# Kernel tuning notes

Measured on AMD Instinct MI355X. Metric: run time of the kernel, lower is better.

## Reference

```python
import jax, jax.numpy as jnp
import numpy as np

B, L, C, H, D2 = 1, 384, 256, 8, 128
d = C // H
EPS = 1e-5
SCALE = 1.0 / np.sqrt(d).astype(np.float32)


def setup_inputs() -> dict:
    key = jax.random.key(0)
    ks = jax.random.split(key, 20)

    def lin(k, fin, fout):
        return (jax.random.normal(k, (fin, fout), jnp.float32) / np.sqrt(fin)).astype(jnp.float32)

    return {
        "x2d": jax.random.normal(ks[0], (B, L, L, D2), jnp.float32),
        "x3d": jax.random.normal(ks[1], (B, L, C), jnp.float32),
        "Wq": lin(ks[2], C, C), "bq": jax.random.normal(ks[3], (C,), jnp.float32) * 0.02,
        "Wk": lin(ks[4], C, C), "bk": jax.random.normal(ks[5], (C,), jnp.float32) * 0.02,
        "Wv": lin(ks[6], C, C), "bv": jax.random.normal(ks[7], (C,), jnp.float32) * 0.02,
        "Wpre": lin(ks[8], D2, C), "bpre": jax.random.normal(ks[9], (C,), jnp.float32) * 0.02,
        "ln_g": jnp.ones((C,), jnp.float32), "ln_b": jnp.zeros((C,), jnp.float32),
        "Weq": lin(ks[10], C, C), "beq": jax.random.normal(ks[11], (C,), jnp.float32) * 0.02,
        "Wek": lin(ks[12], C, C), "bek": jax.random.normal(ks[13], (C,), jnp.float32) * 0.02,
        "Wo": lin(ks[14], C, C), "bo": jax.random.normal(ks[15], (C,), jnp.float32) * 0.02,
    }


def reference(x2d, x3d, Wq, bq, Wk, bk, Wv, bv, Wpre, bpre, ln_g, ln_b,
              Weq, beq, Wek, bek, Wo, bo):
    def heads(x):  # (B,L,C) -> (B,H,L,d)
        return x.reshape(B, L, H, d).transpose(0, 2, 1, 3)

    q = heads(x3d @ Wq + bq)
    k = heads(x3d @ Wk + bk)
    v = heads(x3d @ Wv + bv)

    # pre_proj: Linear -> LayerNorm -> ReLU on pair features
    e = x2d @ Wpre + bpre                              # (B,L,L,C)
    mu = jnp.mean(e, axis=-1, keepdims=True)
    var = jnp.mean((e - mu) ** 2, axis=-1, keepdims=True)
    e = jax.nn.relu((e - mu) * jax.lax.rsqrt(var + EPS) * ln_g + ln_b)

    efq = (e @ Weq + beq).reshape(B, L, L, H, d)       # efq[b,i,j,h,:]
    efk = (e @ Wek + bek).reshape(B, L, L, H, d)

    # scores[b,h,i,j] = q_i.k_j + sum_d efk[b,i,j,h,d]*q[b,h,j,d], then scale
    scores = jnp.einsum('bhid,bhjd->bhij', q, k) \
           + jnp.einsum('bijhd,bhjd->bhij', efk, q)
    scores = scores * SCALE

    w = jax.nn.softmax(scores, axis=-1)
    x1 = jnp.einsum('bhij,bhjd->bhid', w, v)
    # x2[b,h,i,d] = sum_j scores[b,h,i,j] * efq[b,i,j,h,d]
    x2 = jnp.einsum('bhij,bijhd->bhid', scores, efq)

    x = (x1 + x2).transpose(0, 2, 1, 3).reshape(B, L, C)
    return x @ Wo + bo
```

## Files before the change

kernel.cpp:

```cpp
#include <hip/hip_runtime.h>
#include <hip/hip_bf16.h>

#define LLEN 384
#define CDIM 256
#define NH 8
#define HD 32
#define DIN 128
#define LN_EPS 1e-5f
#define SCL 0.17677669529663687f

typedef __attribute__((ext_vector_type(8))) short bh8;
typedef __attribute__((ext_vector_type(4))) float f32x4;
typedef __attribute__((ext_vector_type(4))) unsigned int u32x4;

__device__ __forceinline__ unsigned short f2bf(float f){
  unsigned int u = __float_as_uint(f);
  u += 0x7fffu + ((u >> 16) & 1u);
  return (unsigned short)(u >> 16);
}

__device__ __forceinline__ unsigned int pkbf(float a, float b){
#if defined(__gfx950__) && __has_builtin(__builtin_amdgcn_cvt_pk_bf16_f32)
  typedef __attribute__((ext_vector_type(2))) __bf16 vbf2;
  vbf2 v = __builtin_amdgcn_cvt_pk_bf16_f32(a, b);
  union { vbf2 v; unsigned int u; } cv; cv.v = v; return cv.u;
#else
  return (unsigned int)f2bf(a) | ((unsigned int)f2bf(b) << 16);
#endif
}

__device__ __forceinline__ float pk_reduce8(const float* v, int lane){
  bool b0 = lane & 1, b1 = lane & 2, b2 = lane & 4;
  float r0 = (b0 ? v[1] : v[0]) + __shfl_xor(b0 ? v[0] : v[1], 1, 64);
  float r1 = (b0 ? v[3] : v[2]) + __shfl_xor(b0 ? v[2] : v[3], 1, 64);
  float r2 = (b0 ? v[5] : v[4]) + __shfl_xor(b0 ? v[4] : v[5], 1, 64);
  float r3 = (b0 ? v[7] : v[6]) + __shfl_xor(b0 ? v[6] : v[7], 1, 64);
  float s0 = (b1 ? r1 : r0) + __shfl_xor(b1 ? r0 : r1, 2, 64);
  float s1 = (b1 ? r3 : r2) + __shfl_xor(b1 ? r2 : r3, 2, 64);
  float t0 = (b2 ? s1 : s0) + __shfl_xor(b2 ? s0 : s1, 4, 64);
  return t0 + __shfl_xor(t0, 8, 64);
}

__global__ __launch_bounds__(256) void pack_w(
    const float* __restrict__ Wpre, const float* __restrict__ Weq,
    const float* __restrict__ Wek,  const float* __restrict__ Wq,
    const float* __restrict__ Wk,   const float* __restrict__ Wv,
    unsigned short* __restrict__ Pp, unsigned short* __restrict__ Pq,
    unsigned short* __restrict__ Pk, unsigned short* __restrict__ PWq,
    unsigned short* __restrict__ PWk, unsigned short* __restrict__ PWv)
{
  int tid = blockIdx.x * 256 + threadIdx.x;
  const float* W; unsigned short* P; int base;
  if      (tid <  4096){ W = Wpre; P = Pp;  base = tid;         }
  else if (tid < 12288){ W = Weq;  P = Pq;  base = tid -  4096; }
  else if (tid < 20480){ W = Wek;  P = Pk;  base = tid - 12288; }
  else if (tid < 28672){ W = Wq;   P = PWq; base = tid - 20480; }
  else if (tid < 36864){ W = Wk;   P = PWk; base = tid - 28672; }
  else                 { W = Wv;   P = PWv; base = tid - 36864; }
  int l   = base & 63;
  int c   = (base >> 6) & 15;
  int kc  = base >> 10;
  int krow = kc*32 + (l >> 4)*8;
  int col  = c*16 + (l & 15);
  unsigned int wds[4];
  #pragma unroll
  for (int p = 0; p < 4; p++){
    unsigned short lo = f2bf(W[(size_t)(krow + 2*p    )*CDIM + col]);
    unsigned short hi = f2bf(W[(size_t)(krow + 2*p + 1)*CDIM + col]);
    wds[p] = (unsigned int)lo | ((unsigned int)hi << 16);
  }
  uint4 v; v.x = wds[0]; v.y = wds[1]; v.z = wds[2]; v.w = wds[3];
  *(uint4*)(P + (size_t)base*8) = v;
}

__global__ __launch_bounds__(256) void qkv_mfma(
    const float* __restrict__ x3d,
    const float* __restrict__ bq, const float* __restrict__ bk, const float* __restrict__ bv,
    const unsigned short* __restrict__ PWq, const unsigned short* __restrict__ PWk,
    const unsigned short* __restrict__ PWv,
    float* __restrict__ Vm, unsigned short* __restrict__ QmH,
    float* __restrict__ QmT, unsigned short* __restrict__ PKt)
{
  __shared__ __align__(16) unsigned short Xb[64*264];
  const int bx = blockIdx.x;
  const int jb = bx / 12, rem = bx % 12;
  const int m = rem >> 2, nq = rem & 3;
  const int t  = threadIdx.x;
  const int w  = t >> 6, l = t & 63, q4 = l >> 4, lm = l & 15;

  const float* src = x3d + (size_t)jb*64*CDIM;
  #pragma unroll
  for (int it = 0; it < 16; it++){
    int idx = it*256 + t;
    int r = idx >> 6, k4 = (idx & 63) << 2;
    float4 v = *(const float4*)(src + (size_t)r*CDIM + k4);
    ushort4 b;
    b.x = f2bf(v.x); b.y = f2bf(v.y); b.z = f2bf(v.z); b.w = f2bf(v.w);
    *(ushort4*)(&Xb[r*264 + k4]) = b;
  }
  __syncthreads();

  const unsigned short* P = (m == 0) ? PWq : (m == 1) ? PWk : PWv;
  const float* bias       = (m == 0) ? bq  : (m == 1) ? bk  : bv;
  const int cidx = nq*4 + w;
  f32x4 acc[4];
  #pragma unroll
  for (int a = 0; a < 4; a++){ f32x4 z = {0.f,0.f,0.f,0.f}; acc[a] = z; }
  #pragma unroll
  for (int kc = 0; kc < 8; kc++){
    bh8 bf = *(const bh8*)(P + ((size_t)(kc*16 + cidx)*64 + l)*8);
    #pragma unroll
    for (int rt = 0; rt < 4; rt++){
      bh8 af = *(const bh8*)(&Xb[(rt*16 + lm)*264 + kc*32 + q4*8]);
      acc[rt] = __builtin_amdgcn_mfma_f32_16x16x32_bf16(af, bf, acc[rt], 0, 0, 0);
    }
  }
  {
    int c = cidx*16 + lm;
    float bb = bias[c];
    #pragma unroll
    for (int rt = 0; rt < 4; rt++)
      #pragma unroll
      for (int rg = 0; rg < 4; rg++){
        int row = jb*64 + rt*16 + q4*4 + rg;
        float v = acc[rt][rg] + bb;
        if (m == 0){
          QmH[(size_t)row*CDIM + c] = f2bf(v);
          QmT[(size_t)c*LLEN + row] = v;
        } else if (m == 1){
          int kc2 = c >> 5;
          int jj2 = c & 7;
          int l2  = ((c >> 3) & 3)*16 + (row & 15);
          PKt[(((size_t)kc2*24 + (row >> 4))*64 + l2)*8 + jj2] = f2bf(v);
        } else {
          Vm[(size_t)row*CDIM + c] = v;
        }
      }
  }
}

__global__ __launch_bounds__(256, 4) void x3d_tiles(
  const float* __restrict__ x2d,
  const float* __restrict__ bpre, const float* __restrict__ ln_g, const float* __restrict__ ln_b,
  const float* __restrict__ beq,  const float* __restrict__ bek,
  const float* __restrict__ QmT,  const unsigned short* __restrict__ QmH,
  const unsigned short* __restrict__ PKt,
  const unsigned short* __restrict__ Pp, const unsigned short* __restrict__ Pq,
  const unsigned short* __restrict__ Pk,
  float* __restrict__ Sg, float* __restrict__ x2part)
{
  __shared__ __align__(16) unsigned short EX[64*264];
  __shared__ float rowstat[4][64][2];
  __shared__ float muS[64], istdS[64];
  __shared__ float qk1S[NH*64];

  const int bx = blockIdx.x;
  const int i = bx / 6, jt = bx % 6, j0 = jt * 64;
  const int t = threadIdx.x;
  const int w = t >> 6, l = t & 63, q4 = l >> 4, lm = l & 15;
  const int wbase = w << 6;

  bh8 aqv[2], kf[2][4];
  #pragma unroll
  for (int hh = 0; hh < 2; hh++){
    int h = 2*w + hh;
    aqv[hh] = *(const bh8*)(QmH + (size_t)i*CDIM + h*HD + q4*8);
    #pragma unroll
    for (int ct = 0; ct < 4; ct++)
      kf[hh][ct] = *(const bh8*)(PKt + (((size_t)h*24 + (jt*4 + ct))*64 + l)*8);
  }

  {
    const char* gtile = (const char*)(x2d + ((size_t)i*LLEN + j0)*DIN);
    #pragma unroll
    for (int it = 0; it < 8; it++){
      int P   = w*512 + it*64 + l;
      int row = P >> 5;
      int blk = (P & 31) ^ (row & 7);
      const void* gp = gtile + ((size_t)row*512 + ((size_t)blk << 4));
      unsigned short* lp = EX + (w*4096 + it*512);
      __builtin_amdgcn_global_load_lds(
          (const __attribute__((address_space(1))) void*)gp,
          (__attribute__((address_space(3))) void*)lp, 16, 0, 0);
    }
  }

  #pragma unroll
  for (int hh = 0; hh < 2; hh++){
    int h = 2*w + hh;
    #pragma unroll
    for (int ct = 0; ct < 4; ct++){
      f32x4 z = {0.f,0.f,0.f,0.f};
      f32x4 a1 = __builtin_amdgcn_mfma_f32_16x16x32_bf16(aqv[hh], kf[hh][ct], z, 0, 0, 0);
      if (q4 == 0) qk1S[h*64 + ct*16 + lm] = a1[0];
    }
  }

  __syncthreads();

  const float* XF = (const float*)EX;
  f32x4 acc[4][4];
  #pragma unroll
  for (int a = 0; a < 4; a++)
    #pragma unroll
    for (int b = 0; b < 4; b++){ f32x4 z = {0.f,0.f,0.f,0.f}; acc[a][b] = z; }
  #pragma unroll
  for (int kc = 0; kc < 4; kc++){
    bh8 af[4];
    #pragma unroll
    for (int rt = 0; rt < 4; rt++){
      int row = rt*16 + lm;
      int sw  = row & 7;
      int blk0 = kc*8 + q4*2;
      f32x4 a0 = *(const f32x4*)(XF + row*128 + ((blk0       ^ sw) << 2));
      f32x4 a1 = *(const f32x4*)(XF + row*128 + (((blk0 + 1) ^ sw) << 2));
      union { unsigned int u[4]; bh8 v; } cv;
      cv.u[0] = pkbf(a0[0], a0[1]); cv.u[1] = pkbf(a0[2], a0[3]);
      cv.u[2] = pkbf(a1[0], a1[1]); cv.u[3] = pkbf(a1[2], a1[3]);
      af[rt] = cv.v;
    }
    #pragma unroll
    for (int ct = 0; ct < 4; ct++){
      bh8 bf = *(const bh8*)(Pp + ((size_t)(kc*16 + (w*4 + ct))*64 + l)*8);
      #pragma unroll
      for (int rt = 0; rt < 4; rt++)
        acc[rt][ct] = __builtin_amdgcn_mfma_f32_16x16x32_bf16(af[rt], bf, acc[rt][ct], 0, 0, 0);
    }
  }

  {
    float bpre4[4];
    #pragma unroll
    for (int ct = 0; ct < 4; ct++) bpre4[ct] = bpre[wbase + ct*16 + lm];
    #pragma unroll
    for (int rt = 0; rt < 4; rt++){
      float v[8];
      #pragma unroll
      for (int p = 0; p < 8; p++) v[p] = 0.f;
      #pragma unroll
      for (int ct = 0; ct < 4; ct++){
        float bb = bpre4[ct];
        #pragma unroll
        for (int rg = 0; rg < 4; rg++){
          float x = acc[rt][ct][rg] + bb;
          acc[rt][ct][rg] = x;
          v[2*rg]   += x;
          v[2*rg+1] += x*x;
        }
      }
      float red = pk_reduce8(v, lm);
      if (lm < 8){
        int p = lm;
        rowstat[w][rt*16 + q4*4 + (p >> 1)][p & 1] = red;
      }
    }
  }
  __syncthreads();
  if (t < 64){
    float s  = rowstat[0][t][0] + rowstat[1][t][0] + rowstat[2][t][0] + rowstat[3][t][0];
    float s2 = rowstat[0][t][1] + rowstat[1][t][1] + rowstat[2][t][1] + rowstat[3][t][1];
    float mu = s * (1.f/256.f);
    float var = s2 * (1.f/256.f) - mu*mu;
    muS[t] = mu;
    istdS[t] = rsqrtf(var + LN_EPS);
  }
  __syncthreads();

  {
    float g4[4], lb4[4];
    #pragma unroll
    for (int ct = 0; ct < 4; ct++){
      int c = wbase + ct*16 + lm;
      g4[ct] = ln_g[c]; lb4[ct] = ln_b[c];
    }
    #pragma unroll
    for (int rt = 0; rt < 4; rt++){
      #pragma unroll
      for (int rg = 0; rg < 4; rg++){
        int row = rt*16 + q4*4 + rg;
        float mu = muS[row], is = istdS[row];
        #pragma unroll
        for (int ct = 0; ct < 4; ct++){
          int c = wbase + ct*16 + lm;
          float v = (acc[rt][ct][rg] - mu)*is*g4[ct] + lb4[ct];
          v = fmaxf(v, 0.f);
          EX[row*264 + c] = f2bf(v);
        }
      }
    }
  }
  __syncthreads();

  #pragma unroll
  for (int a = 0; a < 4; a++)
    #pragma unroll
    for (int b = 0; b < 4; b++){ f32x4 z = {0.f,0.f,0.f,0.f}; acc[a][b] = z; }
  #pragma unroll
  for (int kc = 0; kc < 8; kc++){
    bh8 af[4];
    #pragma unroll
    for (int rt = 0; rt < 4; rt++)
      af[rt] = *(const bh8*)(&EX[(rt*16 + lm)*264 + kc*32 + q4*8]);
    #pragma unroll
    for (int ct = 0; ct < 4; ct++){
      bh8 bf = *(const bh8*)(Pk + ((size_t)(kc*16 + (w*4 + ct))*64 + l)*8);
      #pragma unroll
      for (int rt = 0; rt < 4; rt++)
        acc[rt][ct] = __builtin_amdgcn_mfma_f32_16x16x32_bf16(af[rt], bf, acc[rt][ct], 0, 0, 0);
    }
  }

  float screg[4];
  {
    float bek4[4];
    #pragma unroll
    for (int ct = 0; ct < 4; ct++) bek4[ct] = bek[wbase + ct*16 + lm];
    #pragma unroll
    for (int rt = 0; rt < 4; rt++){
      float v[8];
      #pragma unroll
      for (int p = 0; p < 8; p++) v[p] = 0.f;
      #pragma unroll
      for (int ct = 0; ct < 4; ct++){
        float bek_ = bek4[ct];
        float4 qv = *(const float4*)(QmT + (size_t)(wbase + ct*16 + lm)*LLEN + j0 + rt*16 + q4*4);
        int wh = ct >> 1;
        v[0 + wh] += (acc[rt][ct][0] + bek_) * qv.x;
        v[2 + wh] += (acc[rt][ct][1] + bek_) * qv.y;
        v[4 + wh] += (acc[rt][ct][2] + bek_) * qv.z;
        v[6 + wh] += (acc[rt][ct][3] + bek_) * qv.w;
      }
      float red = pk_reduce8(v, lm);
      int p = lm & 7;
      int jloc = rt*16 + q4*4 + (p >> 1);
      float sc = (red + qk1S[(2*w + (p & 1))*64 + jloc]) * SCL;
      screg[rt] = sc;
      if (lm < 8)
        Sg[((size_t)i*NH + 2*w + (p & 1))*LLEN + j0 + jloc] = sc;
    }
  }

  #pragma unroll
  for (int a = 0; a < 4; a++)
    #pragma unroll
    for (int b = 0; b < 4; b++){ f32x4 z = {0.f,0.f,0.f,0.f}; acc[a][b] = z; }
  #pragma unroll
  for (int kc = 0; kc < 8; kc++){
    bh8 af[4];
    #pragma unroll
    for (int rt = 0; rt < 4; rt++)
      af[rt] = *(const bh8*)(&EX[(rt*16 + lm)*264 + kc*32 + q4*8]);
    #pragma unroll
    for (int ct = 0; ct < 4; ct++){
      bh8 bf = *(const bh8*)(Pq + ((size_t)(kc*16 + (w*4 + ct))*64 + l)*8);
      #pragma unroll
      for (int rt = 0; rt < 4; rt++)
        acc[rt][ct] = __builtin_amdgcn_mfma_f32_16x16x32_bf16(af[rt], bf, acc[rt][ct], 0, 0, 0);
    }
  }

  {
    float beq4[4];
    #pragma unroll
    for (int ct = 0; ct < 4; ct++) beq4[ct] = beq[wbase + ct*16 + lm];
    float x2p[4] = {0.f, 0.f, 0.f, 0.f};
    #pragma unroll
    for (int rt = 0; rt < 4; rt++){
      float sb[8];
      #pragma unroll
      for (int p = 0; p < 8; p++)
        sb[p] = __shfl(screg[rt], (l & 48) | p, 64);
      #pragma unroll
      for (int ct = 0; ct < 4; ct++){
        int wh = ct >> 1;
        #pragma unroll
        for (int rg = 0; rg < 4; rg++)
          x2p[ct] = fmaf(sb[2*rg + wh], acc[rt][ct][rg] + beq4[ct], x2p[ct]);
      }
    }
    bool b4 = l & 16, b5 = l & 32;
    float r0 = (b4 ? x2p[1] : x2p[0]) + __shfl_xor(b4 ? x2p[0] : x2p[1], 16, 64);
    float r1 = (b4 ? x2p[3] : x2p[2]) + __shfl_xor(b4 ? x2p[2] : x2p[3], 16, 64);
    float q  = (b5 ? r1 : r0) + __shfl_xor(b5 ? r0 : r1, 32, 64);
    int ctq = ((l >> 4) & 1) | (((l >> 5) & 1) << 1);
    x2part[((size_t)jt*LLEN + i)*CDIM + wbase + ctq*16 + lm] = q;
  }
}

__global__ __launch_bounds__(256) void finish(
    const float* __restrict__ Sg, const float* __restrict__ x2part,
    const float* __restrict__ Vm, const float* __restrict__ Wo,
    const float* __restrict__ bo, float* __restrict__ out)
{
  __shared__ float scoresS[NH*LLEN];
  __shared__ float xoutS[CDIM];
  const int i = blockIdx.x;
  const int t = threadIdx.x;

  #pragma unroll
  for (int it = 0; it < 3; it++)
    ((float4*)scoresS)[it*256 + t] = ((const float4*)(Sg + (size_t)i*NH*LLEN))[it*256 + t];
  __syncthreads();

  const int h = t >> 5;
  const int g32 = t & 31;
  float sv[12];
  float mx = -3.0e38f;
  #pragma unroll
  for (int it = 0; it < 12; it++){
    float s = scoresS[h*LLEN + it*32 + g32];
    sv[it] = s;
    mx = fmaxf(mx, s);
  }
  #pragma unroll
  for (int mk = 1; mk < 32; mk <<= 1) mx = fmaxf(mx, __shfl_xor(mx, mk, 64));
  float den = 0.f;
  #pragma unroll
  for (int it = 0; it < 12; it++){ float e = __expf(sv[it] - mx); sv[it] = e; den += e; }
  #pragma unroll
  for (int mk = 1; mk < 32; mk <<= 1) den += __shfl_xor(den, mk, 64);
  float rden = 1.f / den;
  #pragma unroll
  for (int it = 0; it < 12; it++) scoresS[h*LLEN + it*32 + g32] = sv[it]*rden;
  __syncthreads();

  float a[8];
  #pragma unroll
  for (int k = 0; k < 8; k++) a[k] = 0.f;
  {
    const float* vp = Vm + t;
    const float* sp = scoresS + h*LLEN;
    #pragma unroll 2
    for (int j = 0; j < LLEN; j += 8){
      #pragma unroll
      for (int k = 0; k < 8; k++)
        a[k] = fmaf(sp[j+k], vp[(size_t)(j+k)*CDIM], a[k]);
    }
  }
  float x1 = ((a[0]+a[1]) + (a[2]+a[3])) + ((a[4]+a[5]) + (a[6]+a[7]));
  float x2v = 0.f;
  #pragma unroll
  for (int jt = 0; jt < 6; jt++)
    x2v += x2part[((size_t)jt*LLEN + i)*CDIM + t];
  xoutS[t] = x1 + x2v;
  __syncthreads();

  float b0a = bo[t], b1a = 0.f, b2a = 0.f, b3a = 0.f;
  #pragma unroll 4
  for (int c = 0; c < CDIM; c += 4){
    b0a = fmaf(xoutS[c+0], Wo[(size_t)(c+0)*CDIM + t], b0a);
    b1a = fmaf(xoutS[c+1], Wo[(size_t)(c+1)*CDIM + t], b1a);
    b2a = fmaf(xoutS[c+2], Wo[(size_t)(c+2)*CDIM + t], b2a);
    b3a = fmaf(xoutS[c+3], Wo[(size_t)(c+3)*CDIM + t], b3a);
  }
  out[(size_t)i*CDIM + t] = (b0a + b1a) + (b2a + b3a);
}

extern "C" void kernel_launch(void* const* d_in, const int* in_sizes, int n_in,
                              void* d_out, int out_size, void* d_ws, size_t ws_size,
                              hipStream_t stream)
{
  const float* x2d  = (const float*)d_in[0];
  const float* x3d  = (const float*)d_in[1];
  const float* Wq   = (const float*)d_in[2];
  const float* bq   = (const float*)d_in[3];
  const float* Wk   = (const float*)d_in[4];
  const float* bk   = (const float*)d_in[5];
  const float* Wv   = (const float*)d_in[6];
  const float* bv   = (const float*)d_in[7];
  const float* Wpre = (const float*)d_in[8];
  const float* bpre = (const float*)d_in[9];
  const float* ln_g = (const float*)d_in[10];
  const float* ln_b = (const float*)d_in[11];
  const float* Weq  = (const float*)d_in[12];
  const float* beq  = (const float*)d_in[13];
  const float* Wek  = (const float*)d_in[14];
  const float* bek  = (const float*)d_in[15];
  const float* Wo   = (const float*)d_in[16];
  const float* bo   = (const float*)d_in[17];
  float* out = (float*)d_out;

  float* Vm  = (float*)d_ws;
  float* QmT = Vm + LLEN*CDIM;
  unsigned short* QmH = (unsigned short*)(QmT + CDIM*LLEN);
  unsigned short* PKt = QmH + LLEN*CDIM;
  unsigned short* Pp  = PKt + LLEN*CDIM;
  unsigned short* Pq  = Pp  + DIN*CDIM;
  unsigned short* Pk  = Pq  + CDIM*CDIM;
  unsigned short* PWq = Pk  + CDIM*CDIM;
  unsigned short* PWk = PWq + CDIM*CDIM;
  unsigned short* PWv = PWk + CDIM*CDIM;
  float* Sg     = (float*)(PWv + CDIM*CDIM);
  float* x2part = Sg + (size_t)LLEN*NH*LLEN;

  pack_w<<<dim3(176), dim3(256), 0, stream>>>(Wpre, Weq, Wek, Wq, Wk, Wv,
                                              Pp, Pq, Pk, PWq, PWk, PWv);
  qkv_mfma<<<dim3(72), dim3(256), 0, stream>>>(x3d, bq, bk, bv, PWq, PWk, PWv,
                                               Vm, QmH, QmT, PKt);
  x3d_tiles<<<dim3(LLEN*6), dim3(256), 0, stream>>>(x2d, bpre, ln_g, ln_b, beq, bek,
                                                    QmT, QmH, PKt, Pp, Pq, Pk, Sg, x2part);
  finish<<<dim3(LLEN), dim3(256), 0, stream>>>(Sg, x2part, Vm, Wo, bo, out);
}
```

Before: 236.5 us.

## Make x3d_tiles persistent with double-buffered LDS prefetch of next x2d tile

```diff
diff --git a/kernel.cpp b/kernel.cpp
--- a/kernel.cpp
+++ b/kernel.cpp
@@ -11,7 +11,6 @@
 
 typedef __attribute__((ext_vector_type(8))) short bh8;
 typedef __attribute__((ext_vector_type(4))) float f32x4;
-typedef __attribute__((ext_vector_type(4))) unsigned int u32x4;
 
 __device__ __forceinline__ unsigned short f2bf(float f){
   unsigned int u = __float_as_uint(f);
@@ -139,7 +138,7 @@
   }
 }
 
-__global__ __launch_bounds__(256, 4) void x3d_tiles(
+__global__ __launch_bounds__(256, 2) void x3d_tiles(
   const float* __restrict__ x2d,
   const float* __restrict__ bpre, const float* __restrict__ ln_g, const float* __restrict__ ln_b,
   const float* __restrict__ beq,  const float* __restrict__ bek,
@@ -149,89 +148,107 @@
   const unsigned short* __restrict__ Pk,
   float* __restrict__ Sg, float* __restrict__ x2part)
 {
-  __shared__ __align__(16) unsigned short EX[64*264];
+  __shared__ __align__(16) unsigned short BUF[2][64*256];
   __shared__ float rowstat[4][64][2];
   __shared__ float muS[64], istdS[64];
   __shared__ float qk1S[NH*64];
 
-  const int bx = blockIdx.x;
-  const int i = bx / 6, jt = bx % 6, j0 = jt * 64;
+  const int b = blockIdx.x;
   const int t = threadIdx.x;
   const int w = t >> 6, l = t & 63, q4 = l >> 4, lm = l & 15;
   const int wbase = w << 6;
 
-  bh8 aqv[2], kf[2][4];
-  #pragma unroll
-  for (int hh = 0; hh < 2; hh++){
-    int h = 2*w + hh;
-    aqv[hh] = *(const bh8*)(QmH + (size_t)i*CDIM + h*HD + q4*8);
-    #pragma unroll
-    for (int ct = 0; ct < 4; ct++)
-      kf[hh][ct] = *(const bh8*)(PKt + (((size_t)h*24 + (jt*4 + ct))*64 + l)*8);
-  }
-
-  {
-    const char* gtile = (const char*)(x2d + ((size_t)i*LLEN + j0)*DIN);
+  auto stage_tile = [&](int T, unsigned short* dst){
+    const int ii = T / 6, jj0 = (T % 6) * 64;
+    const char* gtile = (const char*)(x2d + ((size_t)ii*LLEN + jj0)*DIN);
     #pragma unroll
     for (int it = 0; it < 8; it++){
       int P   = w*512 + it*64 + l;
       int row = P >> 5;
       int blk = (P & 31) ^ (row & 7);
       const void* gp = gtile + ((size_t)row*512 + ((size_t)blk << 4));
-      unsigned short* lp = EX + (w*4096 + it*512);
+      unsigned short* lp = dst + (w*4096 + it*512);
       __builtin_amdgcn_global_load_lds(
           (const __attribute__((address_space(1))) void*)gp,
           (__attribute__((address_space(3))) void*)lp, 16, 0, 0);
     }
-  }
-
-  #pragma unroll
-  for (int hh = 0; hh < 2; hh++){
-    int h = 2*w + hh;
+  };
+
+  stage_tile(b, &BUF[0][0]);
+
+  int cur = 0;
+  #pragma unroll 1
+  for (int T = b; T < LLEN*6; T += 512){
+    const int i = T / 6, jt = T % 6, j0 = jt * 64;
+    unsigned short* EXs = &BUF[cur][0];
+    unsigned short* ENs = &BUF[cur ^ 1][0];
+
+    __syncthreads();
+
+    bh8 aqv[2], kf[2][4];
+    #pragma unroll
+    for (int hh = 0; hh < 2; hh++){
+      int h = 2*w + hh;
+      aqv[hh] = *(const bh8*)(QmH + (size_t)i*CDIM + h*HD + q4*8);
+      #pragma unroll
+      for (int ct = 0; ct < 4; ct++)
+        kf[hh][ct] = *(const bh8*)(PKt + (((size_t)h*24 + (jt*4 + ct))*64 + l)*8);
+    }
+    bh8 bfp[4][4];
+    #pragma unroll
+    for (int kc = 0; kc < 4; kc++)
+      #pragma unroll
+      for (int ct = 0; ct < 4; ct++)
+        bfp[kc][ct] = *(const bh8*)(Pp + ((size_t)(kc*16 + (w*4 + ct))*64 + l)*8);
+    float bpre4[4], g4[4], lb4[4];
     #pragma unroll
     for (int ct = 0; ct < 4; ct++){
-      f32x4 z = {0.f,0.f,0.f,0.f};
-      f32x4 a1 = __builtin_amdgcn_mfma_f32_16x16x32_bf16(aqv[hh], kf[hh][ct], z, 0, 0, 0);
-      if (q4 == 0) qk1S[h*64 + ct*16 + lm] = a1[0];
-    }
-  }
-
-  __syncthreads();
-
-  const float* XF = (const float*)EX;
-  f32x4 acc[4][4];
-  #pragma unroll
-  for (int a = 0; a < 4; a++)
-    #pragma unroll
-    for (int b = 0; b < 4; b++){ f32x4 z = {0.f,0.f,0.f,0.f}; acc[a][b] = z; }
-  #pragma unroll
-  for (int kc = 0; kc < 4; kc++){
-    bh8 af[4];
-    #pragma unroll
-    for (int rt = 0; rt < 4; rt++){
-      int row = rt*16 + lm;
-      int sw  = row & 7;
-      int blk0 = kc*8 + q4*2;
-      f32x4 a0 = *(const f32x4*)(XF + row*128 + ((blk0       ^ sw) << 2));
-      f32x4 a1 = *(const f32x4*)(XF + row*128 + (((blk0 + 1) ^ sw) << 2));
-      union { unsigned int u[4]; bh8 v; } cv;
-      cv.u[0] = pkbf(a0[0], a0[1]); cv.u[1] = pkbf(a0[2], a0[3]);
-      cv.u[2] = pkbf(a1[0], a1[1]); cv.u[3] = pkbf(a1[2], a1[3]);
-      af[rt] = cv.v;
-    }
-    #pragma unroll
-    for (int ct = 0; ct < 4; ct++){
-      bh8 bf = *(const bh8*)(Pp + ((size_t)(kc*16 + (w*4 + ct))*64 + l)*8);
-      #pragma unroll
-      for (int rt = 0; rt < 4; rt++)
-        acc[rt][ct] = __builtin_amdgcn_mfma_f32_16x16x32_bf16(af[rt], bf, acc[rt][ct], 0, 0, 0);
-    }
-  }
-
-  {
-    float bpre4[4];
-    #pragma unroll
-    for (int ct = 0; ct < 4; ct++) bpre4[ct] = bpre[wbase + ct*16 + lm];
+      int c = wbase + ct*16 + lm;
+      bpre4[ct] = bpre[c]; g4[ct] = ln_g[c]; lb4[ct] = ln_b[c];
+    }
+
+    if (T + 512 < LLEN*6) stage_tile(T + 512, ENs);
+
+    #pragma unroll
+    for (int hh = 0; hh < 2; hh++){
+      int h = 2*w + hh;
+      #pragma unroll
+      for (int ct = 0; ct < 4; ct++){
+        f32x4 z = {0.f,0.f,0.f,0.f};
+        f32x4 a1 = __builtin_amdgcn_mfma_f32_16x16x32_bf16(aqv[hh], kf[hh][ct], z, 0, 0, 0);
+        if (q4 == 0) qk1S[h*64 + ct*16 + lm] = a1[0];
+      }
+    }
+
+    const float* XF = (const float*)EXs;
+    f32x4 acc[4][4];
+    #pragma unroll
+    for (int a = 0; a < 4; a++)
+      #pragma unroll
+      for (int bb2 = 0; bb2 < 4; bb2++){ f32x4 z = {0.f,0.f,0.f,0.f}; acc[a][bb2] = z; }
+    #pragma unroll
+    for (int kc = 0; kc < 4; kc++){
+      bh8 af[4];
+      #pragma unroll
+      for (int rt = 0; rt < 4; rt++){
+        int row = rt*16 + lm;
+        int sw  = row & 7;
+        int blk0 = kc*8 + q4*2;
+        f32x4 a0 = *(const f32x4*)(XF + row*128 + ((blk0       ^ sw) << 2));
+        f32x4 a1 = *(const f32x4*)(XF + row*128 + (((blk0 + 1) ^ sw) << 2));
+        union { unsigned int u[4]; bh8 v; } cv;
+        cv.u[0] = pkbf(a0[0], a0[1]); cv.u[1] = pkbf(a0[2], a0[3]);
+        cv.u[2] = pkbf(a1[0], a1[1]); cv.u[3] = pkbf(a1[2], a1[3]);
+        af[rt] = cv.v;
+      }
+      #pragma unroll
+      for (int ct = 0; ct < 4; ct++){
+        #pragma unroll
+        for (int rt = 0; rt < 4; rt++)
+          acc[rt][ct] = __builtin_amdgcn_mfma_f32_16x16x32_bf16(af[rt], bfp[kc][ct], acc[rt][ct], 0, 0, 0);
+      }
+    }
+
     #pragma unroll
     for (int rt = 0; rt < 4; rt++){
       float v[8];
@@ -254,136 +271,132 @@
         rowstat[w][rt*16 + q4*4 + (p >> 1)][p & 1] = red;
       }
     }
-  }
-  __syncthreads();
-  if (t < 64){
-    float s  = rowstat[0][t][0] + rowstat[1][t][0] + rowstat[2][t][0] + rowstat[3][t][0];
-    float s2 = rowstat[0][t][1] + rowstat[1][t][1] + rowstat[2][t][1] + rowstat[3][t][1];
-    float mu = s * (1.f/256.f);
-    float var = s2 * (1.f/256.f) - mu*mu;
-    muS[t] = mu;
-    istdS[t] = rsqrtf(var + LN_EPS);
-  }
-  __syncthreads();
-
-  {
-    float g4[4], lb4[4];
-    #pragma unroll
-    for (int ct = 0; ct < 4; ct++){
-      int c = wbase + ct*16 + lm;
-      g4[ct] = ln_g[c]; lb4[ct] = ln_b[c];
-    }
+    __syncthreads();
+    if (t < 64){
+      float s  = rowstat[0][t][0] + rowstat[1][t][0] + rowstat[2][t][0] + rowstat[3][t][0];
+      float s2 = rowstat[0][t][1] + rowstat[1][t][1] + rowstat[2][t][1] + rowstat[3][t][1];
+      float mu = s * (1.f/256.f);
+      float var = s2 * (1.f/256.f) - mu*mu;
+      muS[t] = mu;
+      istdS[t] = rsqrtf(var + LN_EPS);
+    }
+    __syncthreads();
+
     #pragma unroll
     for (int rt = 0; rt < 4; rt++){
       #pragma unroll
       for (int rg = 0; rg < 4; rg++){
         int row = rt*16 + q4*4 + rg;
         float mu = muS[row], is = istdS[row];
+        int rsw = row & 7;
         #pragma unroll
         for (int ct = 0; ct < 4; ct++){
           int c = wbase + ct*16 + lm;
           float v = (acc[rt][ct][rg] - mu)*is*g4[ct] + lb4[ct];
           v = fmaxf(v, 0.f);
-          EX[row*264 + c] = f2bf(v);
+          int blk = (c >> 3) ^ rsw;
+          EXs[row*256 + (blk << 3) + (lm & 7)] = f2bf(v);
         }
       }
     }
-  }
-  __syncthreads();
-
-  #pragma unroll
-  for (int a = 0; a < 4; a++)
-    #pragma unroll
-    for (int b = 0; b < 4; b++){ f32x4 z = {0.f,0.f,0.f,0.f}; acc[a][b] = z; }
-  #pragma unroll
-  for (int kc = 0; kc < 8; kc++){
-    bh8 af[4];
-    #pragma unroll
-    for (int rt = 0; rt < 4; rt++)
-      af[rt] = *(const bh8*)(&EX[(rt*16 + lm)*264 + kc*32 + q4*8]);
-    #pragma unroll
-    for (int ct = 0; ct < 4; ct++){
-      bh8 bf = *(const bh8*)(Pk + ((size_t)(kc*16 + (w*4 + ct))*64 + l)*8);
+    __syncthreads();
+
+    #pragma unroll
+    for (int a = 0; a < 4; a++)
+      #pragma unroll
+      for (int bb2 = 0; bb2 < 4; bb2++){ f32x4 z = {0.f,0.f,0.f,0.f}; acc[a][bb2] = z; }
+    #pragma unroll
+    for (int kc = 0; kc < 8; kc++){
+      bh8 af[4];
       #pragma unroll
       for (int rt = 0; rt < 4; rt++)
-        acc[rt][ct] = __builtin_amdgcn_mfma_f32_16x16x32_bf16(af[rt], bf, acc[rt][ct], 0, 0, 0);
-    }
-  }
-
-  float screg[4];
-  {
-    float bek4[4];
-    #pragma unroll
-    for (int ct = 0; ct < 4; ct++) bek4[ct] = bek[wbase + ct*16 + lm];
-    #pragma unroll
-    for (int rt = 0; rt < 4; rt++){
-      float v[8];
-      #pragma unroll
-      for (int p = 0; p < 8; p++) v[p] = 0.f;
+        af[rt] = *(const bh8*)(&EXs[(rt*16 + lm)*256 + (((kc*4 + q4) ^ (lm & 7)) << 3)]);
       #pragma unroll
       for (int ct = 0; ct < 4; ct++){
-        float bek_ = bek4[ct];
-        float4 qv = *(const float4*)(QmT + (size_t)(wbase + ct*16 + lm)*LLEN + j0 + rt*16 + q4*4);
-        int wh = ct >> 1;
-        v[0 + wh] += (acc[rt][ct][0] + bek_) * qv.x;
-        v[2 + wh] += (acc[rt][ct][1] + bek_) * qv.y;
-        v[4 + wh] += (acc[rt][ct][2] + bek_) * qv.z;
-        v[6 + wh] += (acc[rt][ct][3] + bek_) * qv.w;
-      }
-      float red = pk_reduce8(v, lm);
-      int p = lm & 7;
-      int jloc = rt*16 + q4*4 + (p >> 1);
-      float sc = (red + qk1S[(2*w + (p & 1))*64 + jloc]) * SCL;
-      screg[rt] = sc;
-      if (lm < 8)
-        Sg[((size_t)i*NH + 2*w + (p & 1))*LLEN + j0 + jloc] = sc;
-    }
-  }
-
-  #pragma unroll
-  for (int a = 0; a < 4; a++)
-    #pragma unroll
-    for (int b = 0; b < 4; b++){ f32x4 z = {0.f,0.f,0.f,0.f}; acc[a][b] = z; }
-  #pragma unroll
-  for (int kc = 0; kc < 8; kc++){
-    bh8 af[4];
-    #pragma unroll
-    for (int rt = 0; rt < 4; rt++)
-      af[rt] = *(const bh8*)(&EX[(rt*16 + lm)*264 + kc*32 + q4*8]);
-    #pragma unroll
-    for (int ct = 0; ct < 4; ct++){
-      bh8 bf = *(const bh8*)(Pq + ((size_t)(kc*16 + (w*4 + ct))*64 + l)*8);
+        bh8 bf = *(const bh8*)(Pk + ((size_t)(kc*16 + (w*4 + ct))*64 + l)*8);
+        #pragma unroll
+        for (int rt = 0; rt < 4; rt++)
+          acc[rt][ct] = __builtin_amdgcn_mfma_f32_16x16x32_bf16(af[rt], bf, acc[rt][ct], 0, 0, 0);
+      }
+    }
+
+    float screg[4];
+    {
+      float bek4[4];
+      #pragma unroll
+      for (int ct = 0; ct < 4; ct++) bek4[ct] = bek[wbase + ct*16 + lm];
+      #pragma unroll
+      for (int rt = 0; rt < 4; rt++){
+        float v[8];
+        #pragma unroll
+        for (int p = 0; p < 8; p++) v[p] = 0.f;
+        #pragma unroll
+        for (int ct = 0; ct < 4; ct++){
+          float bek_ = bek4[ct];
+          float4 qv = *(const float4*)(QmT + (size_t)(wbase + ct*16 + lm)*LLEN + j0 + rt*16 + q4*4);
+          int wh = ct >> 1;
+          v[0 + wh] += (acc[rt][ct][0] + bek_) * qv.x;
+          v[2 + wh] += (acc[rt][ct][1] + bek_) * qv.y;
+          v[4 + wh] += (acc[rt][ct][2] + bek_) * qv.z;
+          v[6 + wh] += (acc[rt][ct][3] + bek_) * qv.w;
+        }
+        float red = pk_reduce8(v, lm);
+        int p = lm & 7;
+        int jloc = rt*16 + q4*4 + (p >> 1);
+        float sc = (red + qk1S[(2*w + (p & 1))*64 + jloc]) * SCL;
+        screg[rt] = sc;
+        if (lm < 8)
+          Sg[((size_t)i*NH + 2*w + (p & 1))*LLEN + j0 + jloc] = sc;
+      }
+    }
+
+    #pragma unroll
+    for (int a = 0; a < 4; a++)
+      #pragma unroll
+      for (int bb2 = 0; bb2 < 4; bb2++){ f32x4 z = {0.f,0.f,0.f,0.f}; acc[a][bb2] = z; }
+    #pragma unroll
+    for (int kc = 0; kc < 8; kc++){
+      bh8 af[4];
       #pragma unroll
       for (int rt = 0; rt < 4; rt++)
-        acc[rt][ct] = __builtin_amdgcn_mfma_f32_16x16x32_bf16(af[rt], bf, acc[rt][ct], 0, 0, 0);
-    }
-  }
-
-  {
-    float beq4[4];
-    #pragma unroll
-    for (int ct = 0; ct < 4; ct++) beq4[ct] = beq[wbase + ct*16 + lm];
-    float x2p[4] = {0.f, 0.f, 0.f, 0.f};
-    #pragma unroll
-    for (int rt = 0; rt < 4; rt++){
-      float sb[8];
-      #pragma unroll
-      for (int p = 0; p < 8; p++)
-        sb[p] = __shfl(screg[rt], (l & 48) | p, 64);
+        af[rt] = *(const bh8*)(&EXs[(rt*16 + lm)*256 + (((kc*4 + q4) ^ (lm & 7)) << 3)]);
       #pragma unroll
       for (int ct = 0; ct < 4; ct++){
-        int wh = ct >> 1;
-        #pragma unroll
-        for (int rg = 0; rg < 4; rg++)
-          x2p[ct] = fmaf(sb[2*rg + wh], acc[rt][ct][rg] + beq4[ct], x2p[ct]);
-      }
-    }
-    bool b4 = l & 16, b5 = l & 32;
-    float r0 = (b4 ? x2p[1] : x2p[0]) + __shfl_xor(b4 ? x2p[0] : x2p[1], 16, 64);
-    float r1 = (b4 ? x2p[3] : x2p[2]) + __shfl_xor(b4 ? x2p[2] : x2p[3], 16, 64);
-    float q  = (b5 ? r1 : r0) + __shfl_xor(b5 ? r0 : r1, 32, 64);
-    int ctq = ((l >> 4) & 1) | (((l >> 5) & 1) << 1);
-    x2part[((size_t)jt*LLEN + i)*CDIM + wbase + ctq*16 + lm] = q;
+        bh8 bf = *(const bh8*)(Pq + ((size_t)(kc*16 + (w*4 + ct))*64 + l)*8);
+        #pragma unroll
+        for (int rt = 0; rt < 4; rt++)
+          acc[rt][ct] = __builtin_amdgcn_mfma_f32_16x16x32_bf16(af[rt], bf, acc[rt][ct], 0, 0, 0);
+      }
+    }
+
+    {
+      float beq4[4];
+      #pragma unroll
+      for (int ct = 0; ct < 4; ct++) beq4[ct] = beq[wbase + ct*16 + lm];
+      float x2p[4] = {0.f, 0.f, 0.f, 0.f};
+      #pragma unroll
+      for (int rt = 0; rt < 4; rt++){
+        float sb[8];
+        #pragma unroll
+        for (int p = 0; p < 8; p++)
+          sb[p] = __shfl(screg[rt], (l & 48) | p, 64);
+        #pragma unroll
+        for (int ct = 0; ct < 4; ct++){
+          int wh = ct >> 1;
+          #pragma unroll
+          for (int rg = 0; rg < 4; rg++)
+            x2p[ct] = fmaf(sb[2*rg + wh], acc[rt][ct][rg] + beq4[ct], x2p[ct]);
+        }
+      }
+      bool b4 = l & 16, b5 = l & 32;
+      float r0 = (b4 ? x2p[1] : x2p[0]) + __shfl_xor(b4 ? x2p[0] : x2p[1], 16, 64);
+      float r1 = (b4 ? x2p[3] : x2p[2]) + __shfl_xor(b4 ? x2p[2] : x2p[3], 16, 64);
+      float q  = (b5 ? r1 : r0) + __shfl_xor(b5 ? r0 : r1, 32, 64);
+      int ctq = ((l >> 4) & 1) | (((l >> 5) & 1) << 1);
+      x2part[((size_t)jt*LLEN + i)*CDIM + wbase + ctq*16 + lm] = q;
+    }
+
+    cur ^= 1;
   }
 }
 
@@ -497,7 +510,7 @@
                                               Pp, Pq, Pk, PWq, PWk, PWv);
   qkv_mfma<<<dim3(72), dim3(256), 0, stream>>>(x3d, bq, bk, bv, PWq, PWk, PWv,
                                                Vm, QmH, QmT, PKt);
-  x3d_tiles<<<dim3(LLEN*6), dim3(256), 0, stream>>>(x2d, bpre, ln_g, ln_b, beq, bek,
-                                                    QmT, QmH, PKt, Pp, Pq, Pk, Sg, x2part);
+  x3d_tiles<<<dim3(512), dim3(256), 0, stream>>>(x2d, bpre, ln_g, ln_b, beq, bek,
+                                                 QmT, QmH, PKt, Pp, Pq, Pk, Sg, x2part);
   finish<<<dim3(LLEN), dim3(256), 0, stream>>>(Sg, x2part, Vm, Wo, bo, out);
 }
```

Measured after the change: 501.2 us. 2.12x slower.
